# Performance work log

Measured on AMD Instinct MI355X. Metric: run time of the kernel, lower is better.

The kernel has to match this reference:

```python
import jax, jax.numpy as jnp
import numpy as np

D_MODEL = 1024
N_HEADS = 16
HEAD_DIM = D_MODEL // N_HEADS
D_C = 128
THETA = 10000.0


def rope_cos_sin(timestamps):
    # timestamps: (B, L) -> cos, sin: (B, L, HEAD_DIM)
    freqs = 1.0 / (THETA ** (jnp.arange(0, HEAD_DIM, 2, dtype=jnp.float32) / HEAD_DIM))
    t = timestamps[..., None] * freqs            # (B, L, HEAD_DIM//2)
    emb = jnp.concatenate([t, t], axis=-1)       # (B, L, HEAD_DIM)
    return jnp.cos(emb), jnp.sin(emb)


def rotate_half(x):
    x1, x2 = jnp.split(x, 2, axis=-1)
    return jnp.concatenate([-x2, x1], axis=-1)


def setup_inputs() -> dict:
    key = jax.random.key(0)
    ks = jax.random.split(key, 10)
    B, L = 2, 2048
    s = 0.02
    return {
        "query": jax.random.normal(ks[0], (B, L, D_MODEL), jnp.float32),
        "timestamps_q": jax.random.uniform(ks[1], (B, L), jnp.float32) * 365.0,
        "timestamps_kv": jax.random.uniform(ks[2], (B, L), jnp.float32) * 365.0,
        "w_kv_c": jax.random.normal(ks[3], (D_MODEL, D_C), jnp.float32) * s,
        "w_kc_up": jax.random.normal(ks[4], (D_C, D_MODEL), jnp.float32) * s,
        "w_vc_up": jax.random.normal(ks[5], (D_C, D_MODEL), jnp.float32) * s,
        "w_qr": jax.random.normal(ks[6], (D_MODEL, D_MODEL), jnp.float32) * s,
        "w_kr": jax.random.normal(ks[7], (D_MODEL, D_MODEL), jnp.float32) * s,
        "w_o": jax.random.normal(ks[8], (D_MODEL, D_MODEL), jnp.float32) * s,
    }


def reference(query, timestamps_q, timestamps_kv, w_kv_c, w_kc_up, w_vc_up, w_qr, w_kr, w_o):
    B, Lq, _ = query.shape
    key_value = query  # self-attention path (key_value defaults to query)
    Lk = key_value.shape[1]

    def heads(x, L):  # (B, L, D) -> (B, H, L, hd)
        return x.reshape(B, L, N_HEADS, HEAD_DIM).transpose(0, 2, 1, 3)

    c_kv = key_value @ w_kv_c                      # (B, Lk, d_c) low-rank KV
    k_c = heads(c_kv @ w_kc_up, Lk)
    v_c = heads(c_kv @ w_vc_up, Lk)
    q_r = heads(query @ w_qr, Lq)
    k_r = heads(key_value @ w_kr, Lk)

    cos_q, _ = rope_cos_sin(timestamps_q)
    cos_k, _ = rope_cos_sin(timestamps_kv)
    cos_q = cos_q[:, None]                          # (B, 1, Lq, hd)
    cos_k = cos_k[:, None]                          # (B, 1, Lk, hd)
    # Faithful to original (which passes cos_k in the `sin` slot):
    q_r = q_r * cos_q + rotate_half(q_r) * cos_k
    k_r = k_r * cos_q + rotate_half(k_r) * cos_k

    scale = HEAD_DIM ** -0.5
    qs = q_r * scale
    attn = jnp.einsum("bhqd,bhkd->bhqk", qs, k_c) + jnp.einsum("bhqd,bhkd->bhqk", qs, k_r)
    attn_weights = jax.nn.softmax(attn, axis=-1)
    out = jnp.einsum("bhqk,bhkd->bhqd", attn_weights, v_c)
    out = out.transpose(0, 2, 1, 3).reshape(B, Lq, D_MODEL)
    return out @ w_o
```

## Files before the change

### kernel.cpp

```cpp
#include <hip/hip_runtime.h>

typedef float          f32x4    __attribute__((ext_vector_type(4)));
typedef float          f32x2    __attribute__((ext_vector_type(2)));
typedef float          float8v  __attribute__((ext_vector_type(8)));
typedef unsigned short ushort8v __attribute__((ext_vector_type(8)));
typedef unsigned short ushort4v __attribute__((ext_vector_type(4)));
typedef __bf16         bf16x8   __attribute__((ext_vector_type(8)));

__device__ __forceinline__ unsigned short f2b(float x) {
  union { __bf16 b; unsigned short u; } v;
  v.b = (__bf16)x;
  return v.u;
}
__device__ __forceinline__ float b2f(unsigned short h) {
  union { unsigned u; float f; } v; v.u = ((unsigned)h) << 16;
  return v.f;
}

__device__ __forceinline__ void g2lds16(const unsigned short* g,
                                        unsigned short* l) {
  __builtin_amdgcn_global_load_lds(
      (const __attribute__((address_space(1))) unsigned int*)g,
      (__attribute__((address_space(3))) unsigned int*)l, 16, 0, 0);
}

__global__ __launch_bounds__(256) void prep_kernel(
    const float* __restrict__ X, unsigned short* __restrict__ Xb, int cvtb,
    int n8,
    const float* __restrict__ w0, unsigned short* __restrict__ t0,
    const float* __restrict__ w1, unsigned short* __restrict__ t1,
    const float* __restrict__ w2, unsigned short* __restrict__ t2,
    const float* __restrict__ w3, unsigned short* __restrict__ t3,
    const float* __restrict__ w4, unsigned short* __restrict__ t4,
    const float* __restrict__ w5, unsigned short* __restrict__ t5,
    const float* __restrict__ tq, const float* __restrict__ tk,
    f32x2* __restrict__ ctab) {
  __shared__ unsigned short T[64 * 72];
  const int tid = threadIdx.x;
  int blk = blockIdx.x;
  if (blk < cvtb) {
    int i = blk * 256 + tid;
    if (i >= n8) return;
    float8v v = reinterpret_cast<const float8v*>(X)[i];
    ushort8v h;
#pragma unroll
    for (int j = 0; j < 8; ++j) h[j] = f2b(v[j]);
    reinterpret_cast<ushort8v*>(Xb)[i] = h;
    return;
  }
  blk -= cvtb;
  if (blk >= 864) {
    int idx = (blk - 864) * 256 + tid;
    int row = idx >> 5, i = idx & 31;
    float f = exp2f(-(float)i * (13.287712379549449f / 32.f));
    f32x2 c;
    c[0] = cosf(tq[row] * f);
    c[1] = cosf(tk[row] * f);
    ctab[idx] = c;
    return;
  }
  const float* W; unsigned short* WT; int K, N, bx, by;
  if (blk < 256)      { W = w0; WT = t0; K = 1024; N = 1024; bx = blk & 15;         by = blk >> 4; }
  else if (blk < 512) { W = w1; WT = t1; K = 1024; N = 1024; bx = (blk - 256) & 15; by = (blk - 256) >> 4; }
  else if (blk < 544) { W = w2; WT = t2; K = 1024; N = 128;  bx = (blk - 512) & 1;  by = (blk - 512) >> 1; }
  else if (blk < 576) { W = w3; WT = t3; K = 128;  N = 1024; bx = (blk - 544) & 15; by = (blk - 544) >> 4; }
  else if (blk < 608) { W = w4; WT = t4; K = 128;  N = 1024; bx = (blk - 576) & 15; by = (blk - 576) >> 4; }
  else                { W = w5; WT = t5; K = 1024; N = 1024; bx = (blk - 608) & 15; by = (blk - 608) >> 4; }
  const int n0 = bx * 64, k0 = by * 64;
#pragma unroll
  for (int it = 0; it < 2; ++it) {
    int c = tid + it * 256;
    int r = c >> 3, cc = c & 7;
    float8v v = *reinterpret_cast<const float8v*>(
        &W[(size_t)(k0 + r) * N + n0 + cc * 8]);
    ushort8v h;
#pragma unroll
    for (int j = 0; j < 8; ++j) h[j] = f2b(v[j]);
    *reinterpret_cast<ushort8v*>(&T[r * 72 + cc * 8]) = h;
  }
  __syncthreads();
#pragma unroll
  for (int it = 0; it < 2; ++it) {
    int c = tid + it * 256;
    int n = c >> 3, kc = c & 7;
    ushort8v y;
#pragma unroll
    for (int j = 0; j < 8; ++j) y[j] = T[(kc * 8 + j) * 72 + n];
    *reinterpret_cast<ushort8v*>(&WT[(size_t)(n0 + n) * K + k0 + kc * 8]) = y;
  }
}

template <int TM, typename CT, bool ACC>
__global__ __launch_bounds__(256) void gemm_bt(
    const unsigned short* __restrict__ A, const unsigned short* __restrict__ Bt,
    CT* __restrict__ C, int M, int N, int K) {
  __shared__ unsigned short As[TM * 64];
  __shared__ unsigned short Bs[128 * 64];
  const int tid = threadIdx.x;
  const int id = blockIdx.x, cpx = gridDim.x >> 3;
  const int swz = (id & 7) * cpx + (id >> 3);
  const int nwx = N / 128;
  const int m0 = (swz / nwx) * TM, n0 = (swz % nwx) * 128;
  const int wave = tid >> 6, lane = tid & 63;
  const int wm = (wave >> 1) * (TM / 2), wn = (wave & 1) * 64;
  const int l16 = lane & 15, quad = lane >> 4;
  constexpr int MI = TM / 32;

  f32x4 acc[MI][4];
#pragma unroll
  for (int i = 0; i < MI; ++i)
#pragma unroll
    for (int j = 0; j < 4; ++j)
#pragma unroll
      for (int r = 0; r < 4; ++r) acc[i][j][r] = 0.f;

  for (int k0 = 0; k0 < K; k0 += 64) {
    __syncthreads();
#pragma unroll
    for (int it = 0; it < TM * 8 / 256; ++it) {
      int c = it * 256 + tid;
      int m = c >> 3, kc = (c & 7) ^ (m & 7);
      g2lds16(&A[(size_t)(m0 + m) * K + k0 + kc * 8], &As[c * 8]);
    }
#pragma unroll
    for (int it = 0; it < 4; ++it) {
      int c = it * 256 + tid;
      int n = c >> 3, kc = (c & 7) ^ (n & 7);
      g2lds16(&Bt[(size_t)(n0 + n) * K + k0 + kc * 8], &Bs[c * 8]);
    }
    __syncthreads();

#pragma unroll
    for (int ks = 0; ks < 2; ++ks) {
      bf16x8 af[MI], bfr[4];
#pragma unroll
      for (int mi = 0; mi < MI; ++mi) {
        int m = wm + mi * 16 + l16;
        af[mi] = *reinterpret_cast<const bf16x8*>(
            &As[(m * 8 + ((ks * 4 + quad) ^ (m & 7))) * 8]);
      }
#pragma unroll
      for (int ni = 0; ni < 4; ++ni) {
        int n = wn + ni * 16 + l16;
        bfr[ni] = *reinterpret_cast<const bf16x8*>(
            &Bs[(n * 8 + ((ks * 4 + quad) ^ (n & 7))) * 8]);
      }
#pragma unroll
      for (int mi = 0; mi < MI; ++mi)
#pragma unroll
        for (int ni = 0; ni < 4; ++ni)
          acc[mi][ni] = __builtin_amdgcn_mfma_f32_16x16x32_bf16(
              af[mi], bfr[ni], acc[mi][ni], 0, 0, 0);
    }
  }

#pragma unroll
  for (int mi = 0; mi < MI; ++mi)
#pragma unroll
    for (int ni = 0; ni < 4; ++ni) {
      int row = m0 + wm + mi * 16 + quad * 4;
      int col = n0 + wn + ni * 16 + l16;
#pragma unroll
      for (int r = 0; r < 4; ++r) {
        size_t idx = (size_t)(row + r) * N + col;
        float val = acc[mi][ni][r];
        if constexpr (sizeof(CT) == 2) {
          if constexpr (ACC) val += b2f(C[idx]);
          C[idx] = f2b(val);
        } else {
          if constexpr (ACC) val += C[idx];
          C[idx] = val;
        }
      }
    }
}

__global__ __launch_bounds__(256) void gemm_fused3(
    const unsigned short* __restrict__ A, const unsigned short* __restrict__ Bt,
    unsigned short* __restrict__ Cq, unsigned short* __restrict__ Ck,
    unsigned short* __restrict__ Cc, const f32x2* __restrict__ ctab, int K) {
  __shared__ unsigned short As[1024 * 8];
  __shared__ unsigned short Bs[1024 * 8];
  const int tid = threadIdx.x;
  const int id = blockIdx.x;
  const int swz = (id & 7) * 68 + (id >> 3);
  const int m0 = (swz / 17) * 128, n0 = (swz % 17) * 128;
  const int wave = tid >> 6, lane = tid & 63;
  const int wm = (wave >> 1) * 64, wn = (wave & 1) * 64;
  const int l16 = lane & 15, quad = lane >> 4;

  f32x4 acc[4][4];
#pragma unroll
  for (int i = 0; i < 4; ++i)
#pragma unroll
    for (int j = 0; j < 4; ++j)
#pragma unroll
      for (int r = 0; r < 4; ++r) acc[i][j][r] = 0.f;

  for (int k0 = 0; k0 < K; k0 += 64) {
    __syncthreads();
#pragma unroll
    for (int it = 0; it < 4; ++it) {
      int c = it * 256 + tid;
      int m = c >> 3, kc = (c & 7) ^ (m & 7);
      g2lds16(&A[(size_t)(m0 + m) * K + k0 + kc * 8], &As[c * 8]);
    }
#pragma unroll
    for (int it = 0; it < 4; ++it) {
      int c = it * 256 + tid;
      int n = c >> 3, kc = (c & 7) ^ (n & 7);
      g2lds16(&Bt[(size_t)(n0 + n) * K + k0 + kc * 8], &Bs[c * 8]);
    }
    __syncthreads();

#pragma unroll
    for (int ks = 0; ks < 2; ++ks) {
      bf16x8 af[4], bfr[4];
#pragma unroll
      for (int mi = 0; mi < 4; ++mi) {
        int m = wm + mi * 16 + l16;
        af[mi] = *reinterpret_cast<const bf16x8*>(
            &As[(m * 8 + ((ks * 4 + quad) ^ (m & 7))) * 8]);
      }
#pragma unroll
      for (int ni = 0; ni < 4; ++ni) {
        int n = wn + ni * 16 + l16;
        bfr[ni] = *reinterpret_cast<const bf16x8*>(
            &Bs[(n * 8 + ((ks * 4 + quad) ^ (n & 7))) * 8]);
      }
#pragma unroll
      for (int mi = 0; mi < 4; ++mi)
#pragma unroll
        for (int ni = 0; ni < 4; ++ni)
          acc[mi][ni] = __builtin_amdgcn_mfma_f32_16x16x32_bf16(
              af[mi], bfr[ni], acc[mi][ni], 0, 0, 0);
    }
  }

  if (n0 < 2048) {
    const bool isq = (n0 < 1024);
    unsigned short* dst = isq ? Cq : Ck;
    const int cb = isq ? 0 : 1024;
    const float s = isq ? 0.18033688011112042f : 1.0f;
#pragma unroll
    for (int mi = 0; mi < 4; ++mi)
#pragma unroll
      for (int r = 0; r < 4; ++r) {
        int row = m0 + wm + mi * 16 + quad * 4 + r;
        const f32x2* crow = &ctab[(size_t)row * 32];
#pragma unroll
        for (int np = 0; np < 2; ++np) {
          f32x2 cc = crow[np * 16 + l16];
          float v1 = acc[mi][np][r], v2 = acc[mi][np + 2][r];
          int col = n0 - cb + wn + np * 16 + l16;
          dst[(size_t)row * 1024 + col]      = f2b((v1 * cc[0] - v2 * cc[1]) * s);
          dst[(size_t)row * 1024 + col + 32] = f2b((v2 * cc[0] + v1 * cc[1]) * s);
        }
      }
  } else {
#pragma unroll
    for (int mi = 0; mi < 4; ++mi)
#pragma unroll
      for (int ni = 0; ni < 4; ++ni) {
        int row = m0 + wm + mi * 16 + quad * 4;
        int col = n0 - 2048 + wn + ni * 16 + l16;
#pragma unroll
        for (int r = 0; r < 4; ++r)
          Cc[(size_t)(row + r) * 128 + col] = f2b(acc[mi][ni][r]);
      }
  }
}

__global__ __launch_bounds__(256) void gemm_fused2(
    const unsigned short* __restrict__ A, const unsigned short* __restrict__ Bt,
    unsigned short* __restrict__ Ck, unsigned short* __restrict__ vt, int K) {
  __shared__ unsigned short As[1024 * 8];
  __shared__ unsigned short Bs[1024 * 8];
  const int tid = threadIdx.x;
  const int id = blockIdx.x;
  const int swz = (id & 7) * 64 + (id >> 3);
  const int m0 = (swz >> 4) * 128, n0 = (swz & 15) * 128;
  const int wave = tid >> 6, lane = tid & 63;
  const int wm = (wave >> 1) * 64, wn = (wave & 1) * 64;
  const int l16 = lane & 15, quad = lane >> 4;

  f32x4 acc[4][4];
#pragma unroll
  for (int i = 0; i < 4; ++i)
#pragma unroll
    for (int j = 0; j < 4; ++j)
#pragma unroll
      for (int r = 0; r < 4; ++r) acc[i][j][r] = 0.f;

  for (int k0 = 0; k0 < K; k0 += 64) {
    __syncthreads();
#pragma unroll
    for (int it = 0; it < 4; ++it) {
      int c = it * 256 + tid;
      int m = c >> 3, kc = (c & 7) ^ (m & 7);
      g2lds16(&A[(size_t)(m0 + m) * K + k0 + kc * 8], &As[c * 8]);
    }
#pragma unroll
    for (int it = 0; it < 4; ++it) {
      int c = it * 256 + tid;
      int n = c >> 3, kc = (c & 7) ^ (n & 7);
      g2lds16(&Bt[(size_t)(n0 + n) * K + k0 + kc * 8], &Bs[c * 8]);
    }
    __syncthreads();

#pragma unroll
    for (int ks = 0; ks < 2; ++ks) {
      bf16x8 af[4], bfr[4];
#pragma unroll
      for (int mi = 0; mi < 4; ++mi) {
        int m = wm + mi * 16 + l16;
        af[mi] = *reinterpret_cast<const bf16x8*>(
            &As[(m * 8 + ((ks * 4 + quad) ^ (m & 7))) * 8]);
      }
#pragma unroll
      for (int ni = 0; ni < 4; ++ni) {
        int n = wn + ni * 16 + l16;
        bfr[ni] = *reinterpret_cast<const bf16x8*>(
            &Bs[(n * 8 + ((ks * 4 + quad) ^ (n & 7))) * 8]);
      }
#pragma unroll
      for (int mi = 0; mi < 4; ++mi)
#pragma unroll
        for (int ni = 0; ni < 4; ++ni)
          acc[mi][ni] = __builtin_amdgcn_mfma_f32_16x16x32_bf16(
              af[mi], bfr[ni], acc[mi][ni], 0, 0, 0);
    }
  }

  if (n0 < 1024) {
#pragma unroll
    for (int mi = 0; mi < 4; ++mi)
#pragma unroll
      for (int ni = 0; ni < 4; ++ni) {
        int row = m0 + wm + mi * 16 + quad * 4;
        int col = n0 + wn + ni * 16 + l16;
#pragma unroll
        for (int r = 0; r < 4; ++r) {
          size_t idx = (size_t)(row + r) * 1024 + col;
          Ck[idx] = f2b(acc[mi][ni][r] + b2f(Ck[idx]));
        }
      }
  } else {
    const int L = 2048;
#pragma unroll
    for (int mi = 0; mi < 4; ++mi)
#pragma unroll
      for (int ni = 0; ni < 4; ++ni) {
        int row = m0 + wm + mi * 16 + quad * 4;
        int col = n0 - 1024 + wn + ni * 16 + l16;
        int l = row & (L - 1);
        int bh = ((row >> 11) << 4) | (col >> 6);
        int d = col & 63;
        int s = (l & ~63) | (((l >> 5) & 1) << 5) | (((l >> 3) & 1) << 4) |
                (((l >> 2) & 1) << 3) | (((l >> 4) & 1) << 2);
        ushort4v w;
#pragma unroll
        for (int r = 0; r < 4; ++r) w[r] = f2b(acc[mi][ni][r]);
        *reinterpret_cast<ushort4v*>(
            &vt[(size_t)bh * 64 * L + (size_t)d * L + s]) = w;
      }
  }
}

__global__ __launch_bounds__(256, 3) void flash17_kernel(
    const unsigned short* __restrict__ qs, const unsigned short* __restrict__ ks,
    const unsigned short* __restrict__ vt, unsigned short* __restrict__ o,
    int L) {
  __shared__ unsigned short Ks[3][512 * 8];
  __shared__ unsigned short Vs[3][512 * 8];
  const int tid = threadIdx.x;
  const int wave = tid >> 6, lane = tid & 63;
  const int l16 = lane & 15, quad = lane >> 4;
  const int bh = blockIdx.y;
  const int qb = blockIdx.x * 128 + wave * 32;
  const size_t base = ((size_t)(bh >> 4) * L) * 1024 + (bh & 15) * 64;
  const size_t vtbase = (size_t)bh * 64 * L;

  bf16x8 aq[2][2];
#pragma unroll
  for (int mt = 0; mt < 2; ++mt) {
    size_t qrow = base + (size_t)(qb + mt * 16 + l16) * 1024;
    aq[mt][0] = *reinterpret_cast<const bf16x8*>(&qs[qrow + quad * 8]);
    aq[mt][1] = *reinterpret_cast<const bf16x8*>(&qs[qrow + 32 + quad * 8]);
  }

  ushort8v onesu;
#pragma unroll
  for (int j = 0; j < 8; ++j) onesu[j] = 0x3F80;
  bf16x8 ones = *reinterpret_cast<bf16x8*>(&onesu);

  f32x4 oacc[2][4];
  f32x4 lacc[2];
#pragma unroll
  for (int mt = 0; mt < 2; ++mt) {
#pragma unroll
    for (int r = 0; r < 4; ++r) lacc[mt][r] = 0.f;
#pragma unroll
    for (int nt = 0; nt < 4; ++nt)
#pragma unroll
      for (int r = 0; r < 4; ++r) oacc[mt][nt][r] = 0.f;
  }

  auto stage = [&](int t, int b) {
    int k0 = t * 64;
#pragma unroll
    for (int it = 0; it < 2; ++it) {
      int c = it * 256 + tid;
      int key = c >> 3, dc = (c & 7) ^ (key & 7);
      g2lds16(&ks[base + (size_t)(k0 + key) * 1024 + dc * 8], &Ks[b][c * 8]);
    }
#pragma unroll
    for (int it = 0; it < 2; ++it) {
      int c = it * 256 + tid;
      int d = c >> 3, kc = (c & 7) ^ (d & 7);
      g2lds16(&vt[vtbase + (size_t)d * L + k0 + kc * 8], &Vs[b][c * 8]);
    }
  };

  const int T = L / 64;
  stage(0, 0);
  stage(1, 1);

  for (int t = 0; t < T; ++t) {
    __builtin_amdgcn_s_barrier();
    asm volatile("" ::: "memory");
    if (t + 2 < T) stage(t + 2, (t + 2) % 3);
    if (t + 2 < T)
      asm volatile("s_waitcnt vmcnt(8)" ::: "memory");
    else if (t + 1 < T)
      asm volatile("s_waitcnt vmcnt(4)" ::: "memory");
    else
      asm volatile("s_waitcnt vmcnt(0)" ::: "memory");
    __builtin_amdgcn_s_barrier();
    asm volatile("" ::: "memory");

    const int cb = t % 3;
    const unsigned short* Kb = &Ks[cb][0];
    const unsigned short* Vb = &Vs[cb][0];

    f32x4 st[2][4];
#pragma unroll
    for (int nt = 0; nt < 4; ++nt) {
      int key = nt * 16 + l16;
      int dc0 = quad ^ (key & 7);
      int dc1 = (4 + quad) ^ (key & 7);
      bf16x8 bk0 = *reinterpret_cast<const bf16x8*>(&Kb[(key * 8 + dc0) * 8]);
      bf16x8 bk1 = *reinterpret_cast<const bf16x8*>(&Kb[(key * 8 + dc1) * 8]);
#pragma unroll
      for (int mt = 0; mt < 2; ++mt) {
        f32x4 z; z[0] = z[1] = z[2] = z[3] = 0.f;
        z = __builtin_amdgcn_mfma_f32_16x16x32_bf16(bk0, aq[mt][0], z, 0, 0, 0);
        z = __builtin_amdgcn_mfma_f32_16x16x32_bf16(bk1, aq[mt][1], z, 0, 0, 0);
        st[mt][nt] = z;
      }
    }

    bf16x8 ap[2][2];
#pragma unroll
    for (int mt = 0; mt < 2; ++mt) {
#pragma unroll
      for (int hf = 0; hf < 2; ++hf)
#pragma unroll
        for (int w = 0; w < 4; ++w) {
          int nt = 2 * hf + (w >> 1), p = w & 1;
          ap[mt][hf][2 * w] =
              (__bf16)__builtin_amdgcn_exp2f(st[mt][nt][2 * p]);
          ap[mt][hf][2 * w + 1] =
              (__bf16)__builtin_amdgcn_exp2f(st[mt][nt][2 * p + 1]);
        }
      lacc[mt] = __builtin_amdgcn_mfma_f32_16x16x32_bf16(ap[mt][0], ones,
                                                         lacc[mt], 0, 0, 0);
      lacc[mt] = __builtin_amdgcn_mfma_f32_16x16x32_bf16(ap[mt][1], ones,
                                                         lacc[mt], 0, 0, 0);
    }

#pragma unroll
    for (int nt = 0; nt < 4; ++nt) {
      int d = nt * 16 + l16;
#pragma unroll
      for (int hf = 0; hf < 2; ++hf) {
        int kc = (hf * 4 + quad) ^ (d & 7);
        bf16x8 bv = *reinterpret_cast<const bf16x8*>(&Vb[(d * 8 + kc) * 8]);
#pragma unroll
        for (int mt = 0; mt < 2; ++mt)
          oacc[mt][nt] = __builtin_amdgcn_mfma_f32_16x16x32_bf16(
              ap[mt][hf], bv, oacc[mt][nt], 0, 0, 0);
      }
    }
  }

#pragma unroll
  for (int mt = 0; mt < 2; ++mt)
#pragma unroll
    for (int r = 0; r < 4; ++r) {
      float inv = __builtin_amdgcn_rcpf(lacc[mt][r]);
      int q = qb + mt * 16 + quad * 4 + r;
#pragma unroll
      for (int nt = 0; nt < 4; ++nt)
        o[base + (size_t)q * 1024 + nt * 16 + l16] =
            f2b(oacc[mt][nt][r] * inv);
    }
}

extern "C" void kernel_launch(void* const* d_in, const int* in_sizes, int n_in,
                              void* d_out, int out_size, void* d_ws, size_t ws_size,
                              hipStream_t stream) {
  const float* X    = (const float*)d_in[0];
  const float* tq   = (const float*)d_in[1];
  const float* tk   = (const float*)d_in[2];
  const float* wkvc = (const float*)d_in[3];
  const float* wkc  = (const float*)d_in[4];
  const float* wvc  = (const float*)d_in[5];
  const float* wqr  = (const float*)d_in[6];
  const float* wkr  = (const float*)d_in[7];
  const float* wo   = (const float*)d_in[8];

  const int D = 1024, DC = 128, L = 2048;
  const int M = in_sizes[0] / D;
  const int B = M / L;
  const int NBH = B * 16;
  (void)n_in; (void)out_size; (void)ws_size;

  unsigned short* p = (unsigned short*)d_ws;
  auto take = [&](size_t n) { unsigned short* r = p; p += n; return r; };
  unsigned short* Xb    = take((size_t)M * D);
  unsigned short* qsb   = take((size_t)M * D);
  unsigned short* ksb   = take((size_t)M * D);
  unsigned short* vcb   = take((size_t)M * D);
  unsigned short* ckv   = take((size_t)M * DC);
  unsigned short* Wbig  = take((size_t)(2 * D + DC) * D);
  unsigned short* Wkcvc = take((size_t)(2 * D) * DC);
  unsigned short* WoT   = take((size_t)D * D);
  f32x2* ctab = (f32x2*)take((size_t)M * 32 * 4);
  unsigned short* vtb   = Xb;
  unsigned short* obuf  = vcb;

  const int n8 = M * D / 8;
  const int cvtb = (n8 + 255) / 256;
  const int ropeb = M / 8;
  prep_kernel<<<cvtb + 864 + ropeb, 256, 0, stream>>>(
      X, Xb, cvtb, n8,
      wqr,  Wbig,
      wkr,  Wbig + (size_t)D * D,
      wkvc, Wbig + (size_t)2 * D * D,
      wkc,  Wkcvc,
      wvc,  Wkcvc + (size_t)D * DC,
      wo,   WoT,
      tq, tk, ctab);

  {
    gemm_fused3<<<(2 * D + DC) / 128 * (M / 128), 256, 0, stream>>>(
        Xb, Wbig, qsb, ksb, ckv, ctab, D);
  }
  {
    gemm_fused2<<<(2 * D / 128) * (M / 128), 256, 0, stream>>>(
        ckv, Wkcvc, ksb, vtb, DC);
  }

  dim3 fg(L / 128, NBH);
  flash17_kernel<<<fg, 256, 0, stream>>>(qsb, ksb, vtb, obuf, L);

  {
    gemm_bt<64, float, false><<<(D / 128) * (M / 64), 256, 0, stream>>>(
        obuf, WoT, (float*)d_out, M, D, D);
  }
}
```

Baseline: 199.3 us.

## Double-buffer LDS tiles in GEMM kernels to overlap global loads with MFMA

```diff
diff --git a/kernel.cpp b/kernel.cpp
--- a/kernel.cpp
+++ b/kernel.cpp
@@ -94,8 +94,9 @@
 __global__ __launch_bounds__(256) void gemm_bt(
     const unsigned short* __restrict__ A, const unsigned short* __restrict__ Bt,
     CT* __restrict__ C, int M, int N, int K) {
-  __shared__ unsigned short As[TM * 64];
-  __shared__ unsigned short Bs[128 * 64];
+  static_assert(TM == 64, "vmcnt literal assumes TM=64");
+  __shared__ unsigned short As[2][TM * 64];
+  __shared__ unsigned short Bs[2][128 * 64];
   const int tid = threadIdx.x;
   const int id = blockIdx.x, cpx = gridDim.x >> 3;
   const int swz = (id & 7) * cpx + (id >> 3);
@@ -114,21 +115,35 @@
 #pragma unroll
       for (int r = 0; r < 4; ++r) acc[i][j][r] = 0.f;
 
-  for (int k0 = 0; k0 < K; k0 += 64) {
-    __syncthreads();
+  auto stage = [&](int k0, int b) {
 #pragma unroll
     for (int it = 0; it < TM * 8 / 256; ++it) {
       int c = it * 256 + tid;
       int m = c >> 3, kc = (c & 7) ^ (m & 7);
-      g2lds16(&A[(size_t)(m0 + m) * K + k0 + kc * 8], &As[c * 8]);
+      g2lds16(&A[(size_t)(m0 + m) * K + k0 + kc * 8], &As[b][c * 8]);
     }
 #pragma unroll
     for (int it = 0; it < 4; ++it) {
       int c = it * 256 + tid;
       int n = c >> 3, kc = (c & 7) ^ (n & 7);
-      g2lds16(&Bt[(size_t)(n0 + n) * K + k0 + kc * 8], &Bs[c * 8]);
-    }
-    __syncthreads();
+      g2lds16(&Bt[(size_t)(n0 + n) * K + k0 + kc * 8], &Bs[b][c * 8]);
+    }
+  };
+
+  const int T = K / 64;
+  stage(0, 0);
+  for (int t = 0; t < T; ++t) {
+    __builtin_amdgcn_s_barrier();
+    asm volatile("" ::: "memory");
+    if (t + 1 < T) {
+      stage((t + 1) * 64, (t + 1) & 1);
+      asm volatile("s_waitcnt vmcnt(6)" ::: "memory");
+    } else {
+      asm volatile("s_waitcnt vmcnt(0)" ::: "memory");
+    }
+    __builtin_amdgcn_s_barrier();
+    asm volatile("" ::: "memory");
+    const int cb = t & 1;
 
 #pragma unroll
     for (int ks = 0; ks < 2; ++ks) {
@@ -137,13 +152,13 @@
       for (int mi = 0; mi < MI; ++mi) {
         int m = wm + mi * 16 + l16;
         af[mi] = *reinterpret_cast<const bf16x8*>(
-            &As[(m * 8 + ((ks * 4 + quad) ^ (m & 7))) * 8]);
+            &As[cb][(m * 8 + ((ks * 4 + quad) ^ (m & 7))) * 8]);
       }
 #pragma unroll
       for (int ni = 0; ni < 4; ++ni) {
         int n = wn + ni * 16 + l16;
         bfr[ni] = *reinterpret_cast<const bf16x8*>(
-            &Bs[(n * 8 + ((ks * 4 + quad) ^ (n & 7))) * 8]);
+            &Bs[cb][(n * 8 + ((ks * 4 + quad) ^ (n & 7))) * 8]);
       }
 #pragma unroll
       for (int mi = 0; mi < MI; ++mi)
@@ -179,8 +194,8 @@
     const unsigned short* __restrict__ A, const unsigned short* __restrict__ Bt,
     unsigned short* __restrict__ Cq, unsigned short* __restrict__ Ck,
     unsigned short* __restrict__ Cc, const f32x2* __restrict__ ctab, int K) {
-  __shared__ unsigned short As[1024 * 8];
-  __shared__ unsigned short Bs[1024 * 8];
+  __shared__ unsigned short As[2][1024 * 8];
+  __shared__ unsigned short Bs[2][1024 * 8];
   const int tid = threadIdx.x;
   const int id = blockIdx.x;
   const int swz = (id & 7) * 68 + (id >> 3);
@@ -197,21 +212,35 @@
 #pragma unroll
       for (int r = 0; r < 4; ++r) acc[i][j][r] = 0.f;
 
-  for (int k0 = 0; k0 < K; k0 += 64) {
-    __syncthreads();
+  auto stage = [&](int k0, int b) {
 #pragma unroll
     for (int it = 0; it < 4; ++it) {
       int c = it * 256 + tid;
       int m = c >> 3, kc = (c & 7) ^ (m & 7);
-      g2lds16(&A[(size_t)(m0 + m) * K + k0 + kc * 8], &As[c * 8]);
+      g2lds16(&A[(size_t)(m0 + m) * K + k0 + kc * 8], &As[b][c * 8]);
     }
 #pragma unroll
     for (int it = 0; it < 4; ++it) {
       int c = it * 256 + tid;
       int n = c >> 3, kc = (c & 7) ^ (n & 7);
-      g2lds16(&Bt[(size_t)(n0 + n) * K + k0 + kc * 8], &Bs[c * 8]);
-    }
-    __syncthreads();
+      g2lds16(&Bt[(size_t)(n0 + n) * K + k0 + kc * 8], &Bs[b][c * 8]);
+    }
+  };
+
+  const int T = K / 64;
+  stage(0, 0);
+  for (int t = 0; t < T; ++t) {
+    __builtin_amdgcn_s_barrier();
+    asm volatile("" ::: "memory");
+    if (t + 1 < T) {
+      stage((t + 1) * 64, (t + 1) & 1);
+      asm volatile("s_waitcnt vmcnt(8)" ::: "memory");
+    } else {
+      asm volatile("s_waitcnt vmcnt(0)" ::: "memory");
+    }
+    __builtin_amdgcn_s_barrier();
+    asm volatile("" ::: "memory");
+    const int cb = t & 1;
 
 #pragma unroll
     for (int ks = 0; ks < 2; ++ks) {
@@ -220,13 +249,13 @@
       for (int mi = 0; mi < 4; ++mi) {
         int m = wm + mi * 16 + l16;
         af[mi] = *reinterpret_cast<const bf16x8*>(
-            &As[(m * 8 + ((ks * 4 + quad) ^ (m & 7))) * 8]);
+            &As[cb][(m * 8 + ((ks * 4 + quad) ^ (m & 7))) * 8]);
       }
 #pragma unroll
       for (int ni = 0; ni < 4; ++ni) {
         int n = wn + ni * 16 + l16;
         bfr[ni] = *reinterpret_cast<const bf16x8*>(
-            &Bs[(n * 8 + ((ks * 4 + quad) ^ (n & 7))) * 8]);
+            &Bs[cb][(n * 8 + ((ks * 4 + quad) ^ (n & 7))) * 8]);
       }
 #pragma unroll
       for (int mi = 0; mi < 4; ++mi)
@@ -274,8 +303,8 @@
 __global__ __launch_bounds__(256) void gemm_fused2(
     const unsigned short* __restrict__ A, const unsigned short* __restrict__ Bt,
     unsigned short* __restrict__ Ck, unsigned short* __restrict__ vt, int K) {
-  __shared__ unsigned short As[1024 * 8];
-  __shared__ unsigned short Bs[1024 * 8];
+  __shared__ unsigned short As[2][1024 * 8];
+  __shared__ unsigned short Bs[2][1024 * 8];
   const int tid = threadIdx.x;
   const int id = blockIdx.x;
   const int swz = (id & 7) * 64 + (id >> 3);
@@ -292,21 +321,35 @@
 #pragma unroll
       for (int r = 0; r < 4; ++r) acc[i][j][r] = 0.f;
 
-  for (int k0 = 0; k0 < K; k0 += 64) {
-    __syncthreads();
+  auto stage = [&](int k0, int b) {
 #pragma unroll
     for (int it = 0; it < 4; ++it) {
       int c = it * 256 + tid;
       int m = c >> 3, kc = (c & 7) ^ (m & 7);
-      g2lds16(&A[(size_t)(m0 + m) * K + k0 + kc * 8], &As[c * 8]);
+      g2lds16(&A[(size_t)(m0 + m) * K + k0 + kc * 8], &As[b][c * 8]);
     }
 #pragma unroll
     for (int it = 0; it < 4; ++it) {
       int c = it * 256 + tid;
       int n = c >> 3, kc = (c & 7) ^ (n & 7);
-      g2lds16(&Bt[(size_t)(n0 + n) * K + k0 + kc * 8], &Bs[c * 8]);
-    }
-    __syncthreads();
+      g2lds16(&Bt[(size_t)(n0 + n) * K + k0 + kc * 8], &Bs[b][c * 8]);
+    }
+  };
+
+  const int T = K / 64;
+  stage(0, 0);
+  for (int t = 0; t < T; ++t) {
+    __builtin_amdgcn_s_barrier();
+    asm volatile("" ::: "memory");
+    if (t + 1 < T) {
+      stage((t + 1) * 64, (t + 1) & 1);
+      asm volatile("s_waitcnt vmcnt(8)" ::: "memory");
+    } else {
+      asm volatile("s_waitcnt vmcnt(0)" ::: "memory");
+    }
+    __builtin_amdgcn_s_barrier();
+    asm volatile("" ::: "memory");
+    const int cb = t & 1;
 
 #pragma unroll
     for (int ks = 0; ks < 2; ++ks) {
@@ -315,13 +358,13 @@
       for (int mi = 0; mi < 4; ++mi) {
         int m = wm + mi * 16 + l16;
         af[mi] = *reinterpret_cast<const bf16x8*>(
-            &As[(m * 8 + ((ks * 4 + quad) ^ (m & 7))) * 8]);
+            &As[cb][(m * 8 + ((ks * 4 + quad) ^ (m & 7))) * 8]);
       }
 #pragma unroll
       for (int ni = 0; ni < 4; ++ni) {
         int n = wn + ni * 16 + l16;
         bfr[ni] = *reinterpret_cast<const bf16x8*>(
-            &Bs[(n * 8 + ((ks * 4 + quad) ^ (n & 7))) * 8]);
+            &Bs[cb][(n * 8 + ((ks * 4 + quad) ^ (n & 7))) * 8]);
       }
 #pragma unroll
       for (int mi = 0; mi < 4; ++mi)
```

Measured after the change: 193.0 us. 3.1% less time.
